# Performance work log

Hardware: AMD Instinct MI355X
Metric: run time of the kernel (lower is better)

## Reference

```python
import jax, jax.numpy as jnp
import numpy as np
import string

# Schema: relation_in entities = [e1, e1, e0], relation_out entities = [e0, e1]
N0, N1 = 1024, 512          # e0, e1 instance counts
IN_SHAPE = (N1, N1, N0)
OUT_SHAPE = (N0, N1)

# Each partition is a list of blocks (input_dims, output_dims); dims of the
# same block are set equal (diagonal), input-only blocks are pooled (summed),
# output-only blocks are broadcast. Cross-product of per-entity set partitions:
# e0 owns {in2, out0}; e1 owns {in0, in1, out1}.
_E0_PARTS = [
    [((2,), (0,))],
    [((2,), ()), ((), (0,))],
]
_E1_PARTS = [
    [((0,), ()), ((1,), ()), ((), (1,))],
    [((0, 1), ()), ((), (1,))],
    [((0,), (1,)), ((1,), ())],
    [((1,), (1,)), ((0,), ())],
    [((0, 1), (1,))],
]
PARTITIONS = [a + b for a in _E0_PARTS for b in _E1_PARTS]  # 10 params


def _term(X, blocks):
    """Fused diag -> pool -> broadcast -> undiag -> reindex as one einsum + broadcast."""
    letters = string.ascii_letters
    in_sub = [''] * X.ndim
    keep = []  # (letter, representative output position) for blocks with input AND output
    for k, (i, o) in enumerate(blocks):
        c = letters[k]
        for d in i:
            in_sub[d] = c
        if i and o:
            keep.append((c, min(o)))
    keep.sort(key=lambda t: t[1])
    # repeated input letters = diagonal; letters absent from output = pooled sum
    Z = jnp.einsum(''.join(in_sub) + '->' + ''.join(c for c, _ in keep), X)
    shape = [1] * len(OUT_SHAPE)
    for c, rep in keep:
        shape[rep] = OUT_SHAPE[rep]
    Y = jnp.broadcast_to(Z.reshape(shape), OUT_SHAPE)
    # undiag: any block with >1 output position lives on the diagonal
    for i, o in blocks:
        o = sorted(o)
        if len(o) > 1:
            rep = o[0]
            for p in o[1:]:
                n = OUT_SHAPE[p]
                idx_rep = jnp.arange(n).reshape([n if q == rep else 1 for q in range(len(OUT_SHAPE))])
                idx_p = jnp.arange(n).reshape([n if q == p else 1 for q in range(len(OUT_SHAPE))])
                Y = Y * (idx_rep == idx_p).astype(Y.dtype)
    return Y


def setup_inputs() -> dict:
    key = jax.random.key(0)
    k1, k2 = jax.random.split(key)
    X = jax.random.normal(k1, IN_SHAPE, dtype=jnp.float32)
    # stdv = 1/sqrt(in_dim) = 1.0 -> uniform(-1, 1), shape (params, in_dim, out_dim)
    weights = jax.random.uniform(k2, (len(PARTITIONS), 1, 1), dtype=jnp.float32, minval=-1.0, maxval=1.0)
    return {"X": X, "weights": weights}


def reference(X, weights):
    Y = jnp.zeros(OUT_SHAPE, dtype=X.dtype)
    for i, blocks in enumerate(PARTITIONS):
        Y = Y + _term(X, blocks) * weights[i].reshape(-1)
    return Y
```

## Files before the change

### kernel.cpp

```cpp
#include <hip/hip_runtime.h>


#define N0 1024
#define N1 512

#define TBK 32
#define NBB 16
#define NAB 8
#define TAK 64
#define NCB 4

#define OFF_A1P 0u
#define OFF_A0P (16u*512u*1024u)
#define OFF_A1S (OFF_A0P + 8u*512u*1024u)
#define OFF_A0S (OFF_A1S + 512u*1024u)
#define OFF_S2  (OFF_A0S + 512u*1024u)
#define OFF_D   (OFF_S2 + 1024u)
#define OFF_R0  (OFF_D + 1024u)
#define OFF_R1  (OFF_R0 + 512u)
#define OFF_DG  (OFF_R1 + 512u)

__global__ __launch_bounds__(256, 2) void k1_stream(const float4* __restrict__ Xv,
                                                    float* __restrict__ ws) {
    float4* a1p = (float4*)(ws + OFF_A1P);
    float4* a0p = (float4*)(ws + OFF_A0P);

    const int id  = blockIdx.x;
    const int cb = id & 3;
    const int bb = (id >> 2) & 15;
    const int ab = id >> 6;
    const int tid = threadIdx.x;
    const int w = tid >> 6;
    const int l = tid & 63;
    const int c4 = cb * 64 + l;
    const int b0 = bb * TBK;

    float4 acc[TBK];
#pragma unroll
    for (int k = 0; k < TBK; k++) acc[k] = make_float4(0.f, 0.f, 0.f, 0.f);

    const int a0w = ab * TAK + w;
    const float4* p = Xv + ((size_t)(a0w * N1 + b0)) * (N0 / 4) + c4;
    float4* a1o = a1p + ((size_t)bb * N1 + a0w) * (N0 / 4) + c4;

    for (int i = 0; i < TAK / 4; i++) {
        float4 s = make_float4(0.f, 0.f, 0.f, 0.f);
#pragma unroll
        for (int k = 0; k < TBK; k++) {
            float4 v = p[(size_t)k * (N0 / 4)];
            acc[k] += v;
            s += v;
        }
        *a1o = s;
        p += (size_t)4 * N1 * (N0 / 4);
        a1o += 4 * (N0 / 4);
    }

    __shared__ float4 lred[3][4][64];
    for (int r = 0; r < TBK / 4; r++) {
        if (w > 0) {
#pragma unroll
            for (int q = 0; q < 4; q++) lred[w - 1][q][l] = acc[4 * r + q];
        }
        __syncthreads();
        if (w == 0) {
#pragma unroll
            for (int q = 0; q < 4; q++) {
                float4 t = acc[4 * r + q];
                t += lred[0][q][l];
                t += lred[1][q][l];
                t += lred[2][q][l];
                a0p[((size_t)ab * N1 + (b0 + 4 * r + q)) * (N0 / 4) + c4] = t;
            }
        }
        __syncthreads();
    }
}

__global__ __launch_bounds__(256) void k2_reduce(float* __restrict__ ws) {
    const int tid = threadIdx.x;
    __shared__ float red[256];
    if (blockIdx.x < N1) {
        const int a = blockIdx.x;
        const float4* a1p = (const float4*)(ws + OFF_A1P);
        float4 s = make_float4(0.f, 0.f, 0.f, 0.f);
#pragma unroll
        for (int t = 0; t < NBB; t++) s += a1p[((size_t)t * N1 + a) * (N0 / 4) + tid];
        ((float4*)(ws + OFF_A1S))[(size_t)a * (N0 / 4) + tid] = s;
        red[tid] = s.x + s.y + s.z + s.w;
        __syncthreads();
        for (int st = 128; st; st >>= 1) { if (tid < st) red[tid] += red[tid + st]; __syncthreads(); }
        if (tid == 0) ws[OFF_R0 + a] = red[0];
    } else {
        const int b = blockIdx.x - N1;
        const float4* a0p = (const float4*)(ws + OFF_A0P);
        float4 s = make_float4(0.f, 0.f, 0.f, 0.f);
#pragma unroll
        for (int t = 0; t < NAB; t++) s += a0p[((size_t)t * N1 + b) * (N0 / 4) + tid];
        ((float4*)(ws + OFF_A0S))[(size_t)b * (N0 / 4) + tid] = s;
        red[tid] = s.x + s.y + s.z + s.w;
        __syncthreads();
        for (int st = 128; st; st >>= 1) { if (tid < st) red[tid] += red[tid + st]; __syncthreads(); }
        if (tid == 0) ws[OFF_R1 + b] = red[0];
    }
}

__global__ __launch_bounds__(256) void k3_misc(const float* __restrict__ X,
                                               float* __restrict__ ws) {
    const int tid = threadIdx.x;
    const int blk = blockIdx.x;
    if (blk < 4) {
        const int c = blk * 256 + tid;
        const float* a1s = ws + OFF_A1S;
        float s = 0.f;
        for (int a = 0; a < N1; a++) s += a1s[(size_t)a * N0 + c];
        ws[OFF_S2 + c] = s;
    } else if (blk < 8) {
        const int c = (blk - 4) * 256 + tid;
        float s = 0.f;
        for (int j = 0; j < N1; j++) s += X[(size_t)j * (N1 * N0 + N0) + c];
        ws[OFF_D + c] = s;
    } else {
        const int jb = (blk - 8) * 4;
        __shared__ float red[256];
        for (int r = 0; r < 4; r++) {
            const int j = jb + r;
            const float* row = X + (size_t)j * (N1 * N0 + N0);
            float pr = row[tid] + row[tid + 256] + row[tid + 512] + row[tid + 768];
            red[tid] = pr;
            __syncthreads();
            for (int st = 128; st; st >>= 1) { if (tid < st) red[tid] += red[tid + st]; __syncthreads(); }
            if (tid == 0) ws[OFF_DG + j] = red[0];
            __syncthreads();
        }
    }
}

__global__ __launch_bounds__(256) void k4_combine(const float* __restrict__ X,
                                                  const float* __restrict__ W,
                                                  const float* __restrict__ ws,
                                                  float* __restrict__ Y) {
    const float* A1S = ws + OFF_A1S;
    const float* A0S = ws + OFF_A0S;
    const float* S2 = ws + OFF_S2;
    const float* D  = ws + OFF_D;
    const float* R0 = ws + OFF_R0;
    const float* R1 = ws + OFF_R1;
    const float* Dg = ws + OFF_DG;

    const int tid = threadIdx.x;
    const int ct = blockIdx.x & 15;
    const int jt = blockIdx.x >> 4;
    const int c0 = ct * 64, j0 = jt * 64;

    __shared__ float red[256];
    float p0 = 0.f, p1 = 0.f;
    for (int i = tid; i < N0; i += 256) { p0 += S2[i]; p1 += D[i]; }
    red[tid] = p0; __syncthreads();
    for (int s = 128; s; s >>= 1) { if (tid < s) red[tid] += red[tid + s]; __syncthreads(); }
    const float total = red[0]; __syncthreads();
    red[tid] = p1; __syncthreads();
    for (int s = 128; s; s >>= 1) { if (tid < s) red[tid] += red[tid + s]; __syncthreads(); }
    const float diag_total = red[0]; __syncthreads();

    const float w0 = W[0], w1 = W[1], w2 = W[2], w3 = W[3], w4 = W[4];
    const float w5 = W[5], w6 = W[6], w7 = W[7], w8 = W[8], w9 = W[9];

    const int cl = tid & 63;
    const int jr = tid >> 6;
    const int c = c0 + cl;
    const float base_c = w0 * S2[c] + w1 * D[c] + w5 * total + w6 * diag_total;

    __shared__ float T[64][65];
#pragma unroll
    for (int m = 0; m < 16; m++) {
        const int jo = jr * 16 + m;
        const int j = j0 + jo;
        const float a1 = A1S[(size_t)j * N0 + c];
        const float a0v = A0S[(size_t)j * N0 + c];
        const float dgv = X[(size_t)j * (N1 * N0 + N0) + c];
        const float y = base_c + w2 * a1 + w3 * a0v + w4 * dgv
                      + w7 * R0[j] + w8 * R1[j] + w9 * Dg[j];
        T[jo][cl] = y;
    }
    __syncthreads();
#pragma unroll
    for (int m = 0; m < 16; m++) {
        const int crow = jr * 16 + m;
        Y[(size_t)(c0 + crow) * N1 + (j0 + cl)] = T[cl][crow];
    }
}

extern "C" void kernel_launch(void* const* d_in, const int* in_sizes, int n_in,
                              void* d_out, int out_size, void* d_ws, size_t ws_size,
                              hipStream_t stream) {
    const float* X = (const float*)d_in[0];
    const float* W = (const float*)d_in[1];
    float* Y = (float*)d_out;
    float* ws = (float*)d_ws;

    k1_stream<<<NCB * NBB * NAB, 256, 0, stream>>>((const float4*)X, ws);
    k2_reduce<<<2 * N1, 256, 0, stream>>>(ws);
    k3_misc<<<8 + N1 / 4, 256, 0, stream>>>(X, ws);
    k4_combine<<<16 * 8, 256, 0, stream>>>(X, W, ws, Y);
}
```

Before: 1.458 ms.

## Restructure streaming reduction tiles, merge misc kernel, compute totals from row sums

The streaming kernel now gives each wave 8 a-rows and keeps those per-row accumulators in registers, while the b-row partial sums are reduced across waves through shared memory in groups of four. This cuts register pressure (occupancy rises from 2 to 4 blocks per SM), and X is read with nontemporal loads. The misc kernel is folded into the reduce kernel to save a launch. The column sum S2 is now computed inside the combine kernel, and the grand totals are taken from the existing row-sum vectors R0 and Dg instead of separate column reductions. In exchange, the number of a-blocks doubles, so the a0 partial buffer and its reduction traffic grow, and the combine kernel repeats the S2 column pass in every block.

```diff
diff --git a/kernel.cpp b/kernel.cpp
--- a/kernel.cpp
+++ b/kernel.cpp
@@ -6,24 +6,26 @@
 
 #define TBK 32
 #define NBB 16
-#define NAB 8
-#define TAK 64
+#define TAK 32
+#define NAB 16
 #define NCB 4
+#define BG  4
+
+typedef float f4 __attribute__((ext_vector_type(4)));
 
 #define OFF_A1P 0u
 #define OFF_A0P (16u*512u*1024u)
-#define OFF_A1S (OFF_A0P + 8u*512u*1024u)
+#define OFF_A1S (OFF_A0P + 16u*512u*1024u)
 #define OFF_A0S (OFF_A1S + 512u*1024u)
-#define OFF_S2  (OFF_A0S + 512u*1024u)
-#define OFF_D   (OFF_S2 + 1024u)
+#define OFF_D   (OFF_A0S + 512u*1024u)
 #define OFF_R0  (OFF_D + 1024u)
 #define OFF_R1  (OFF_R0 + 512u)
 #define OFF_DG  (OFF_R1 + 512u)
 
-__global__ __launch_bounds__(256, 2) void k1_stream(const float4* __restrict__ Xv,
+__global__ __launch_bounds__(256, 4) void k1_stream(const f4* __restrict__ Xv,
                                                     float* __restrict__ ws) {
-    float4* a1p = (float4*)(ws + OFF_A1P);
-    float4* a0p = (float4*)(ws + OFF_A0P);
+    f4* a1p = (f4*)(ws + OFF_A1P);
+    f4* a0p = (f4*)(ws + OFF_A0P);
 
     const int id  = blockIdx.x;
     const int cb = id & 3;
@@ -34,97 +36,76 @@
     const int l = tid & 63;
     const int c4 = cb * 64 + l;
     const int b0 = bb * TBK;
+    const int a0w = ab * TAK + w * 8;
 
-    float4 acc[TBK];
+    f4 acc[8];
 #pragma unroll
-    for (int k = 0; k < TBK; k++) acc[k] = make_float4(0.f, 0.f, 0.f, 0.f);
+    for (int i = 0; i < 8; i++) acc[i] = (f4){0.f, 0.f, 0.f, 0.f};
 
-    const int a0w = ab * TAK + w;
-    const float4* p = Xv + ((size_t)(a0w * N1 + b0)) * (N0 / 4) + c4;
-    float4* a1o = a1p + ((size_t)bb * N1 + a0w) * (N0 / 4) + c4;
+    __shared__ f4 lred[3][BG][64];
 
-    for (int i = 0; i < TAK / 4; i++) {
-        float4 s = make_float4(0.f, 0.f, 0.f, 0.f);
+    const f4* pw = Xv + ((size_t)a0w * N1 + b0) * (N0 / 4) + c4;
+
+    for (int g = 0; g < TBK / BG; g++) {
+        f4 s[BG];
 #pragma unroll
-        for (int k = 0; k < TBK; k++) {
-            float4 v = p[(size_t)k * (N0 / 4)];
-            acc[k] += v;
-            s += v;
+        for (int q = 0; q < BG; q++) s[q] = (f4){0.f, 0.f, 0.f, 0.f};
+#pragma unroll
+        for (int i = 0; i < 8; i++) {
+#pragma unroll
+            for (int q = 0; q < BG; q++) {
+                f4 v = __builtin_nontemporal_load(
+                    pw + (size_t)i * N1 * (N0 / 4) + (size_t)(g * BG + q) * (N0 / 4));
+                acc[i] += v;
+                s[q] += v;
+            }
         }
-        *a1o = s;
-        p += (size_t)4 * N1 * (N0 / 4);
-        a1o += 4 * (N0 / 4);
-    }
-
-    __shared__ float4 lred[3][4][64];
-    for (int r = 0; r < TBK / 4; r++) {
         if (w > 0) {
 #pragma unroll
-            for (int q = 0; q < 4; q++) lred[w - 1][q][l] = acc[4 * r + q];
+            for (int q = 0; q < BG; q++) lred[w - 1][q][l] = s[q];
         }
         __syncthreads();
         if (w == 0) {
 #pragma unroll
-            for (int q = 0; q < 4; q++) {
-                float4 t = acc[4 * r + q];
-                t += lred[0][q][l];
-                t += lred[1][q][l];
-                t += lred[2][q][l];
-                a0p[((size_t)ab * N1 + (b0 + 4 * r + q)) * (N0 / 4) + c4] = t;
+            for (int q = 0; q < BG; q++) {
+                f4 t = s[q] + lred[0][q][l] + lred[1][q][l] + lred[2][q][l];
+                a0p[((size_t)ab * N1 + (b0 + g * BG + q)) * (N0 / 4) + c4] = t;
             }
         }
         __syncthreads();
     }
+#pragma unroll
+    for (int i = 0; i < 8; i++)
+        a1p[((size_t)bb * N1 + (a0w + i)) * (N0 / 4) + c4] = acc[i];
 }
 
-__global__ __launch_bounds__(256) void k2_reduce(float* __restrict__ ws) {
+__global__ __launch_bounds__(256) void k2_reduce(const float* __restrict__ X,
+                                                 float* __restrict__ ws) {
     const int tid = threadIdx.x;
+    const int blk = blockIdx.x;
     __shared__ float red[256];
-    if (blockIdx.x < N1) {
-        const int a = blockIdx.x;
-        const float4* a1p = (const float4*)(ws + OFF_A1P);
-        float4 s = make_float4(0.f, 0.f, 0.f, 0.f);
+    if (blk < 2 * N1) {
+        const bool ap = blk < N1;
+        const int r = ap ? blk : blk - N1;
+        const f4* pp = (const f4*)(ws + (ap ? OFF_A1P : OFF_A0P));
+        f4 s = (f4){0.f, 0.f, 0.f, 0.f};
 #pragma unroll
-        for (int t = 0; t < NBB; t++) s += a1p[((size_t)t * N1 + a) * (N0 / 4) + tid];
-        ((float4*)(ws + OFF_A1S))[(size_t)a * (N0 / 4) + tid] = s;
-        red[tid] = s.x + s.y + s.z + s.w;
+        for (int t = 0; t < 16; t++)
+            s += __builtin_nontemporal_load(&pp[((size_t)t * N1 + r) * (N0 / 4) + tid]);
+        ((f4*)(ws + (ap ? OFF_A1S : OFF_A0S)))[(size_t)r * (N0 / 4) + tid] = s;
+        red[tid] = s[0] + s[1] + s[2] + s[3];
         __syncthreads();
         for (int st = 128; st; st >>= 1) { if (tid < st) red[tid] += red[tid + st]; __syncthreads(); }
-        if (tid == 0) ws[OFF_R0 + a] = red[0];
+        if (tid == 0) ws[(ap ? OFF_R0 : OFF_R1) + r] = red[0];
+    } else if (blk < 2 * N1 + 4) {
+        const int c = (blk - 2 * N1) * 256 + tid;
+        float sD = 0.f;
+        for (int j = 0; j < N1; j++) sD += X[(size_t)j * (N1 * N0 + N0) + c];
+        ws[OFF_D + c] = sD;
     } else {
-        const int b = blockIdx.x - N1;
-        const float4* a0p = (const float4*)(ws + OFF_A0P);
-        float4 s = make_float4(0.f, 0.f, 0.f, 0.f);
-#pragma unroll
-        for (int t = 0; t < NAB; t++) s += a0p[((size_t)t * N1 + b) * (N0 / 4) + tid];
-        ((float4*)(ws + OFF_A0S))[(size_t)b * (N0 / 4) + tid] = s;
-        red[tid] = s.x + s.y + s.z + s.w;
-        __syncthreads();
-        for (int st = 128; st; st >>= 1) { if (tid < st) red[tid] += red[tid + st]; __syncthreads(); }
-        if (tid == 0) ws[OFF_R1 + b] = red[0];
-    }
-}
-
-__global__ __launch_bounds__(256) void k3_misc(const float* __restrict__ X,
-                                               float* __restrict__ ws) {
-    const int tid = threadIdx.x;
-    const int blk = blockIdx.x;
-    if (blk < 4) {
-        const int c = blk * 256 + tid;
-        const float* a1s = ws + OFF_A1S;
-        float s = 0.f;
-        for (int a = 0; a < N1; a++) s += a1s[(size_t)a * N0 + c];
-        ws[OFF_S2 + c] = s;
-    } else if (blk < 8) {
-        const int c = (blk - 4) * 256 + tid;
-        float s = 0.f;
-        for (int j = 0; j < N1; j++) s += X[(size_t)j * (N1 * N0 + N0) + c];
-        ws[OFF_D + c] = s;
-    } else {
-        const int jb = (blk - 8) * 4;
-        __shared__ float red[256];
-        for (int r = 0; r < 4; r++) {
-            const int j = jb + r;
+        const int jb = (blk - (2 * N1 + 4)) * 4;
+        for (int r2 = 0; r2 < 4; r2++) {
+            const int j = jb + r2;
             const float* row = X + (size_t)j * (N1 * N0 + N0);
             float pr = row[tid] + row[tid + 256] + row[tid + 512] + row[tid + 768];
             red[tid] = pr;
@@ -142,7 +123,6 @@
                                                   float* __restrict__ Y) {
     const float* A1S = ws + OFF_A1S;
     const float* A0S = ws + OFF_A0S;
-    const float* S2 = ws + OFF_S2;
     const float* D  = ws + OFF_D;
     const float* R0 = ws + OFF_R0;
     const float* R1 = ws + OFF_R1;
@@ -154,12 +134,12 @@
     const int c0 = ct * 64, j0 = jt * 64;
 
     __shared__ float red[256];
-    float p0 = 0.f, p1 = 0.f;
-    for (int i = tid; i < N0; i += 256) { p0 += S2[i]; p1 += D[i]; }
-    red[tid] = p0; __syncthreads();
+    red[tid] = R0[tid] + R0[tid + 256];
+    __syncthreads();
     for (int s = 128; s; s >>= 1) { if (tid < s) red[tid] += red[tid + s]; __syncthreads(); }
     const float total = red[0]; __syncthreads();
-    red[tid] = p1; __syncthreads();
+    red[tid] = Dg[tid] + Dg[tid + 256];
+    __syncthreads();
     for (int s = 128; s; s >>= 1) { if (tid < s) red[tid] += red[tid + s]; __syncthreads(); }
     const float diag_total = red[0]; __syncthreads();
 
@@ -169,7 +149,17 @@
     const int cl = tid & 63;
     const int jr = tid >> 6;
     const int c = c0 + cl;
-    const float base_c = w0 * S2[c] + w1 * D[c] + w5 * total + w6 * diag_total;
+
+    float s2p = 0.f;
+    const float* col = A1S + (size_t)jr * 128 * N0 + c;
+#pragma unroll 8
+    for (int a = 0; a < 128; a++) s2p += col[(size_t)a * N0];
+    __shared__ float s2sh[4][64];
+    s2sh[jr][cl] = s2p;
+    __syncthreads();
+    const float S2c = s2sh[0][cl] + s2sh[1][cl] + s2sh[2][cl] + s2sh[3][cl];
+
+    const float base_c = w0 * S2c + w1 * D[c] + w5 * total + w6 * diag_total;
 
     __shared__ float T[64][65];
 #pragma unroll
@@ -199,8 +189,7 @@
     float* Y = (float*)d_out;
     float* ws = (float*)d_ws;
 
-    k1_stream<<<NCB * NBB * NAB, 256, 0, stream>>>((const float4*)X, ws);
-    k2_reduce<<<2 * N1, 256, 0, stream>>>(ws);
-    k3_misc<<<8 + N1 / 4, 256, 0, stream>>>(X, ws);
+    k1_stream<<<NCB * NBB * NAB, 256, 0, stream>>>((const f4*)X, ws);
+    k2_reduce<<<2 * N1 + 4 + N1 / 4, 256, 0, stream>>>(X, ws);
     k4_combine<<<16 * 8, 256, 0, stream>>>(X, W, ws, Y);
 }
```

Result: slower. 1.506 ms (+3.2%).
